# Kernel optimization log

Hardware: AMD Instinct MI355X
Metric: run time of the kernel (lower is better)

Reference implementation:

```python
import jax, jax.numpy as jnp
import numpy as np

N_NODES = 100000
N_EDGES = 1600000
IN_DIM, HID_DIM, OUT_DIM = 128, 128, 64


def setup_inputs() -> dict:
    key = jax.random.key(0)
    k1, k2, k3, k4, k5, k6, k7 = jax.random.split(key, 7)
    in_feat = jax.random.normal(k1, (N_NODES, IN_DIM), dtype=jnp.float32)
    src = jax.random.randint(k2, (N_EDGES,), 0, N_NODES, dtype=jnp.int32)
    dst = jax.random.randint(k3, (N_EDGES,), 0, N_NODES, dtype=jnp.int32)
    # GraphConv params (Glorot-style scale)
    W1 = jax.random.normal(k4, (IN_DIM, HID_DIM), dtype=jnp.float32) * (2.0 / (IN_DIM + HID_DIM)) ** 0.5
    b1 = jnp.zeros((HID_DIM,), dtype=jnp.float32)
    W2 = jax.random.normal(k5, (HID_DIM, OUT_DIM), dtype=jnp.float32) * (2.0 / (HID_DIM + OUT_DIM)) ** 0.5
    b2 = jnp.zeros((OUT_DIM,), dtype=jnp.float32)
    return {"in_feat": in_feat, "W1": W1, "b1": b1, "W2": W2, "b2": b2, "src": src, "dst": dst}


def _graph_conv(x, W, b, src, dst, inv_sqrt_out, inv_sqrt_in):
    # DGL GraphConv, norm='both': D_out^{-1/2} on source, sum-aggregate, D_in^{-1/2} on dest
    x = x * inv_sqrt_out[:, None]              # [N, d]
    msg = x[src]                               # gather: [E, d]
    agg = jax.ops.segment_sum(msg, dst, num_segments=x.shape[0])  # scatter-add: [N, d]
    agg = agg * inv_sqrt_in[:, None]
    return agg @ W + b


def reference(in_feat, W1, b1, W2, b2, src, dst):
    N = in_feat.shape[0]
    ones = jnp.ones(src.shape[0], dtype=in_feat.dtype)
    deg_out = jax.ops.segment_sum(ones, src, num_segments=N)
    deg_in = jax.ops.segment_sum(ones, dst, num_segments=N)
    # clamp degree to >= 1 (DGL behavior) before inverse sqrt
    inv_sqrt_out = jnp.maximum(deg_out, 1.0) ** -0.5
    inv_sqrt_in = jnp.maximum(deg_in, 1.0) ** -0.5
    h = _graph_conv(in_feat, W1, b1, src, dst, inv_sqrt_out, inv_sqrt_in)
    h = jax.nn.relu(h)
    h = _graph_conv(h, W2, b2, src, dst, inv_sqrt_out, inv_sqrt_in)
    return h
```

## Files before the change

### kernel.cpp

```cpp
#include <hip/hip_runtime.h>

#define N_NODES 100000
#define N_EDGES 1600000
#define IN_DIM 128
#define HID_DIM 128
#define OUT_DIM 64

#define NB 391
#define GRIDB 256
#define EPB (N_EDGES / GRIDB)

typedef unsigned short ushort_t;
typedef unsigned int uint_t;
typedef __attribute__((ext_vector_type(8))) short bf16x8;
typedef __attribute__((ext_vector_type(4))) float f32x4;

__device__ __forceinline__ float blo(uint_t u) { return __uint_as_float(u << 16); }
__device__ __forceinline__ float bhi(uint_t u) { return __uint_as_float(u & 0xFFFF0000u); }
__device__ __forceinline__ uint_t f2b(float f) {
    uint_t u = __float_as_uint(f);
    uint_t r = u + 0x7FFFu + ((u >> 16) & 1u);
    return r >> 16;
}
__device__ __forceinline__ uint_t pk2(float a, float b) { return f2b(a) | (f2b(b) << 16); }


__global__ __launch_bounds__(256) void histdeg_k(const int* __restrict__ src,
                                                 const int* __restrict__ dst,
                                                 int* __restrict__ dego,
                                                 int* __restrict__ bucketTot) {
    __shared__ int h[NB];
    int t = threadIdx.x, blk = blockIdx.x;
    for (int j = t; j < NB; j += 256) h[j] = 0;
    __syncthreads();
    int e0 = blk * EPB;
    for (int i = e0 + t; i < e0 + EPB; i += 256) {
        atomicAdd(&h[dst[i] >> 8], 1);
        atomicAdd(&dego[src[i]], 1);
    }
    __syncthreads();
    for (int j = t; j < NB; j += 256)
        if (h[j]) atomicAdd(&bucketTot[j], h[j]);
}


__global__ __launch_bounds__(512) void bscan_k(const int* __restrict__ bucketTot,
                                               int* __restrict__ bucketOfs,
                                               int* __restrict__ fill) {
    __shared__ int s[512];
    int t = threadIdx.x;
    int v = (t < NB) ? bucketTot[t] : 0;
    s[t] = v;
    __syncthreads();
    for (int off = 1; off < 512; off <<= 1) {
        int x = (t >= off) ? s[t - off] : 0;
        __syncthreads();
        s[t] += x;
        __syncthreads();
    }
    if (t < NB) {
        int e = s[t] - v;
        bucketOfs[t] = e;
        fill[t] = e;
    }
    if (t == 0) bucketOfs[NB] = N_EDGES;
}


__global__ __launch_bounds__(256) void scat_k(const int* __restrict__ src,
                                              const int* __restrict__ dst,
                                              int* __restrict__ fill,
                                              uint_t* __restrict__ ebuf) {
    __shared__ int lcnt[NB];
    __shared__ int base[NB];
    __shared__ int lpos[NB];
    int t = threadIdx.x, blk = blockIdx.x;
    for (int j = t; j < NB; j += 256) {
        lcnt[j] = 0;
        lpos[j] = 0;
    }
    __syncthreads();
    int e0 = blk * EPB;
    for (int i = e0 + t; i < e0 + EPB; i += 256) atomicAdd(&lcnt[dst[i] >> 8], 1);
    __syncthreads();
    for (int j = t; j < NB; j += 256) {
        int c = lcnt[j];
        base[j] = c ? atomicAdd(&fill[j], c) : 0;
    }
    __syncthreads();
    for (int i = e0 + t; i < e0 + EPB; i += 256) {
        int d = dst[i];
        int b = d >> 8;
        int slot = atomicAdd(&lpos[b], 1);
        ebuf[base[b] + slot] = (uint_t)src[i] | ((uint_t)(d & 255) << 17);
    }
}


__global__ __launch_bounds__(256) void fin_k(const uint_t* __restrict__ ebuf,
                                             const int* __restrict__ bucketOfs,
                                             int* __restrict__ ofs,
                                             int* __restrict__ esrc) {
    __shared__ int cnt[256];
    __shared__ int s[256];
    __shared__ int fil[256];
    int b = blockIdx.x, t = threadIdx.x;
    int e0 = bucketOfs[b];
    int e1 = bucketOfs[b + 1];
    cnt[t] = 0;
    __syncthreads();
    for (int i = e0 + t; i < e1; i += 256) atomicAdd(&cnt[ebuf[i] >> 17], 1);
    __syncthreads();
    int c = cnt[t];
    s[t] = c;
    __syncthreads();
    for (int off = 1; off < 256; off <<= 1) {
        int x = (t >= off) ? s[t - off] : 0;
        __syncthreads();
        s[t] += x;
        __syncthreads();
    }
    int excl = s[t] - c;
    int node = b * 256 + t;
    if (node < N_NODES) ofs[node] = e0 + excl;
    if (b == NB - 1 && t == 0) ofs[N_NODES] = N_EDGES;
    fil[t] = excl;
    __syncthreads();
    for (int i = e0 + t; i < e1; i += 256) {
        uint_t u = ebuf[i];
        int slot = atomicAdd(&fil[u >> 17], 1);
        esrc[e0 + slot] = (int)(u & 0x1FFFFu);
    }
}


__global__ __launch_bounds__(256) void prepw_k(const float* __restrict__ x,
                                               const int* __restrict__ dego,
                                               ushort_t* __restrict__ xs,
                                               const float* __restrict__ W1,
                                               const float* __restrict__ W2,
                                               ushort_t* __restrict__ Wf1,
                                               ushort_t* __restrict__ Wf2) {
    constexpr int NB_PREP = N_NODES * 16 / 256;
    if ((int)blockIdx.x < NB_PREP) {
        int gid = blockIdx.x * 256 + threadIdx.x;
        int row = gid >> 4;
        float s = rsqrtf(fmaxf((float)dego[row], 1.0f));
        const float4* xp = (const float4*)x + (size_t)gid * 2;
        float4 va = xp[0], vb = xp[1];
        ((uint4*)xs)[gid] = make_uint4(pk2(va.x * s, va.y * s), pk2(va.z * s, va.w * s),
                                       pk2(vb.x * s, vb.y * s), pk2(vb.z * s, vb.w * s));
        return;
    }
    int gid = (blockIdx.x - NB_PREP) * 256 + threadIdx.x;
    const float* W;
    ushort_t* Wf;
    int BN;
    if (gid < HID_DIM * 16) {
        W = W1; Wf = Wf1; BN = HID_DIM;
    } else {
        gid -= HID_DIM * 16;
        if (gid >= OUT_DIM * 16) return;
        W = W2; Wf = Wf2; BN = OUT_DIM;
    }
    int l = gid & 63;
    int kc = (gid >> 6) & 3;
    int nt = gid >> 8;
    int col = nt * 16 + (l & 15);
    int k0 = kc * 32 + (l >> 4) * 8;
    uint_t r[4];
    #pragma unroll
    for (int p = 0; p < 4; ++p)
        r[p] = pk2(W[(size_t)(k0 + 2 * p) * BN + col], W[(size_t)(k0 + 2 * p + 1) * BN + col]);
    ((uint4*)Wf)[gid] = make_uint4(r[0], r[1], r[2], r[3]);
}

#define ACC8(v)                                         \
    acc[0] += blo(v.x); acc[1] += bhi(v.x);             \
    acc[2] += blo(v.y); acc[3] += bhi(v.y);             \
    acc[4] += blo(v.z); acc[5] += bhi(v.z);             \
    acc[6] += blo(v.w); acc[7] += bhi(v.w);


__global__ __launch_bounds__(256) void agg128_k(const ushort_t* __restrict__ xs,
                                                const int* __restrict__ esrc,
                                                const int* __restrict__ ofs,
                                                ushort_t* __restrict__ a) {
    int wid = (blockIdx.x * 256 + threadIdx.x) >> 6;
    int lane = threadIdx.x & 63;
    int q = lane >> 4, li = lane & 15;
    int beg = ofs[wid], end = ofs[wid + 1];
    float acc[8];
    #pragma unroll
    for (int i = 0; i < 8; ++i) acc[i] = 0.f;

    for (int j = beg; j < end; j += 64) {
        int m = end - j;
        if (m > 64) m = 64;
        int idx = (lane < m) ? esrc[j + lane] : 0;
        for (int t = 0; 4 * t < m; t += 4) {
            int e0 = 4 * t + q, e1 = e0 + 4, e2 = e0 + 8, e3 = e0 + 12;
            int s0 = __shfl(idx, e0 & 63);
            int s1 = __shfl(idx, e1 & 63);
            int s2 = __shfl(idx, e2 & 63);
            int s3 = __shfl(idx, e3 & 63);
            uint4 v0 = *(const uint4*)(xs + (size_t)s0 * 128 + li * 8);
            uint4 v1 = *(const uint4*)(xs + (size_t)s1 * 128 + li * 8);
            uint4 v2 = *(const uint4*)(xs + (size_t)s2 * 128 + li * 8);
            uint4 v3 = *(const uint4*)(xs + (size_t)s3 * 128 + li * 8);
            if (e0 < m) { ACC8(v0) }
            if (e1 < m) { ACC8(v1) }
            if (e2 < m) { ACC8(v2) }
            if (e3 < m) { ACC8(v3) }
        }
    }
    #pragma unroll
    for (int i = 0; i < 8; ++i) acc[i] += __shfl(acc[i], lane ^ 16);
    #pragma unroll
    for (int i = 0; i < 8; ++i) acc[i] += __shfl(acc[i], lane ^ 32);

    if (lane < 16) {
        float sc = rsqrtf(fmaxf((float)(end - beg), 1.0f));
        *(uint4*)(a + (size_t)wid * 128 + li * 8) =
            make_uint4(pk2(acc[0] * sc, acc[1] * sc), pk2(acc[2] * sc, acc[3] * sc),
                       pk2(acc[4] * sc, acc[5] * sc), pk2(acc[6] * sc, acc[7] * sc));
    }
}


__global__ __launch_bounds__(256) void mgemm12_k(const ushort_t* __restrict__ A,
                                                 const ushort_t* __restrict__ Wf1,
                                                 const ushort_t* __restrict__ Wf2,
                                                 const float* __restrict__ b1,
                                                 const int* __restrict__ dego,
                                                 ushort_t* __restrict__ ys) {
    __shared__ ushort_t Hs[4][16][136];
    int wv = threadIdx.x >> 6;
    int l = threadIdx.x & 63;
    int r0 = (blockIdx.x * 4 + wv) * 16;
    if (r0 >= N_NODES) return;
    int q = l >> 4, li = l & 15;

    const ushort_t* ap = A + (size_t)(r0 + li) * 128 + q * 8;
    bf16x8 af[4];
    #pragma unroll
    for (int kc = 0; kc < 4; ++kc) af[kc] = *(const bf16x8*)(ap + kc * 32);

    f32x4 acc[8];
    #pragma unroll
    for (int nt = 0; nt < 8; ++nt) acc[nt] = (f32x4){0.f, 0.f, 0.f, 0.f};

    #pragma unroll
    for (int kc = 0; kc < 4; ++kc) {
        #pragma unroll
        for (int nt = 0; nt < 8; ++nt) {
            bf16x8 bfr = *(const bf16x8*)(Wf1 + ((size_t)(nt * 4 + kc) * 64 + l) * 8);
            acc[nt] = __builtin_amdgcn_mfma_f32_16x16x32_bf16(af[kc], bfr, acc[nt], 0, 0, 0);
        }
    }

    #pragma unroll
    for (int nt = 0; nt < 8; ++nt) {
        float bv = b1[nt * 16 + li];
        #pragma unroll
        for (int j = 0; j < 4; ++j) {
            float x = fmaxf(acc[nt][j] + bv, 0.0f);
            Hs[wv][q * 4 + j][nt * 16 + li] = (ushort_t)f2b(x);
        }
    }

    bf16x8 hf[4];
    #pragma unroll
    for (int kc = 0; kc < 4; ++kc)
        hf[kc] = *(const bf16x8*)&Hs[wv][li][kc * 32 + q * 8];

    f32x4 acc2[4];
    #pragma unroll
    for (int nt = 0; nt < 4; ++nt) acc2[nt] = (f32x4){0.f, 0.f, 0.f, 0.f};

    #pragma unroll
    for (int kc = 0; kc < 4; ++kc) {
        #pragma unroll
        for (int nt = 0; nt < 4; ++nt) {
            bf16x8 bfr = *(const bf16x8*)(Wf2 + ((size_t)(nt * 4 + kc) * 64 + l) * 8);
            acc2[nt] = __builtin_amdgcn_mfma_f32_16x16x32_bf16(hf[kc], bfr, acc2[nt], 0, 0, 0);
        }
    }

    int orow = r0 + q * 4;
    float os[4];
    #pragma unroll
    for (int j = 0; j < 4; ++j) os[j] = rsqrtf(fmaxf((float)dego[orow + j], 1.0f));
    #pragma unroll
    for (int nt = 0; nt < 4; ++nt) {
        #pragma unroll
        for (int j = 0; j < 4; ++j) {
            ys[(size_t)(orow + j) * 64 + nt * 16 + li] = (ushort_t)f2b(acc2[nt][j] * os[j]);
        }
    }
}


__global__ __launch_bounds__(256) void agg64_k(const ushort_t* __restrict__ ys,
                                               const int* __restrict__ esrc,
                                               const int* __restrict__ ofs,
                                               const float* __restrict__ b2,
                                               float* __restrict__ out) {
    int wid = (blockIdx.x * 256 + threadIdx.x) >> 6;
    int lane = threadIdx.x & 63;
    int og = lane >> 3, li = lane & 7;
    int beg = ofs[wid], end = ofs[wid + 1];
    float acc[8];
    #pragma unroll
    for (int i = 0; i < 8; ++i) acc[i] = 0.f;

    for (int j = beg; j < end; j += 64) {
        int m = end - j;
        if (m > 64) m = 64;
        int idx = (lane < m) ? esrc[j + lane] : 0;
        for (int t = 0; 8 * t < m; t += 2) {
            int e0 = 8 * t + og, e1 = e0 + 8;
            int s0 = __shfl(idx, e0 & 63);
            int s1 = __shfl(idx, e1 & 63);
            uint4 v0 = *(const uint4*)(ys + (size_t)s0 * 64 + li * 8);
            uint4 v1 = *(const uint4*)(ys + (size_t)s1 * 64 + li * 8);
            if (e0 < m) { ACC8(v0) }
            if (e1 < m) { ACC8(v1) }
        }
    }
    #pragma unroll
    for (int i = 0; i < 8; ++i) acc[i] += __shfl(acc[i], lane ^ 8);
    #pragma unroll
    for (int i = 0; i < 8; ++i) acc[i] += __shfl(acc[i], lane ^ 16);
    #pragma unroll
    for (int i = 0; i < 8; ++i) acc[i] += __shfl(acc[i], lane ^ 32);

    if (lane < 8) {
        float sc = rsqrtf(fmaxf((float)(end - beg), 1.0f));
        float4 ba = *(const float4*)(b2 + li * 8);
        float4 bb = *(const float4*)(b2 + li * 8 + 4);
        float* op = out + (size_t)wid * 64 + li * 8;
        *(float4*)op = make_float4(acc[0] * sc + ba.x, acc[1] * sc + ba.y,
                                   acc[2] * sc + ba.z, acc[3] * sc + ba.w);
        *(float4*)(op + 4) = make_float4(acc[4] * sc + bb.x, acc[5] * sc + bb.y,
                                         acc[6] * sc + bb.z, acc[7] * sc + bb.w);
    }
}

extern "C" void kernel_launch(void* const* d_in, const int* in_sizes, int n_in,
                              void* d_out, int out_size, void* d_ws, size_t ws_size,
                              hipStream_t stream) {
    const float* in_feat = (const float*)d_in[0];
    const float* W1 = (const float*)d_in[1];
    const float* b1 = (const float*)d_in[2];
    const float* W2 = (const float*)d_in[3];
    const float* b2 = (const float*)d_in[4];
    const int* src = (const int*)d_in[5];
    const int* dst = (const int*)d_in[6];
    float* out = (float*)d_out;

    char* w = (char*)d_ws;
    int* dego = (int*)w;       w += (size_t)N_NODES * 4;
    int* bucketTot = (int*)w;  w += 392 * 4;
    int* fill = (int*)w;       w += 392 * 4;
    int* bucketOfs = (int*)w;  w += 400 * 4;
    int* ofs = (int*)w;        w += (size_t)(N_NODES + 4) * 4;
    uint_t* ebuf = (uint_t*)w; w += (size_t)N_EDGES * 4;
    int* esrc = (int*)w;       w += (size_t)N_EDGES * 4;
    ushort_t* Wf1 = (ushort_t*)w; w += (size_t)HID_DIM * 16 * 16;
    ushort_t* Wf2 = (ushort_t*)w; w += (size_t)OUT_DIM * 16 * 16;
    ushort_t* bufA = (ushort_t*)w; w += (size_t)N_NODES * HID_DIM * 2;
    ushort_t* bufB = (ushort_t*)w; w += (size_t)N_NODES * HID_DIM * 2;

    hipMemsetAsync(dego, 0, (size_t)(N_NODES + 392) * 4, stream);

    histdeg_k<<<GRIDB, 256, 0, stream>>>(src, dst, dego, bucketTot);
    bscan_k<<<1, 512, 0, stream>>>(bucketTot, bucketOfs, fill);
    scat_k<<<GRIDB, 256, 0, stream>>>(src, dst, fill, ebuf);
    fin_k<<<NB, 256, 0, stream>>>(ebuf, bucketOfs, ofs, esrc);

    prepw_k<<<N_NODES * 16 / 256 + 12, 256, 0, stream>>>(in_feat, dego, bufA, W1, W2, Wf1, Wf2);

    agg128_k<<<N_NODES / 4, 256, 0, stream>>>(bufA, esrc, ofs, bufB);

    mgemm12_k<<<(N_NODES / 16 + 3) / 4, 256, 0, stream>>>(bufB, Wf1, Wf2, b1, dego, bufA);

    agg64_k<<<N_NODES / 4, 256, 0, stream>>>(bufA, esrc, ofs, b2, out);
}
```

Baseline: 274.6 us.

## Replace global atomic out-degree count with bucketed source sort in LDS

Out-degree is no longer computed with 1.6M scattered global atomics into dego. Edges are now also bucketed by src>>8 in the histogram and scatter passes, each edge writing a one-byte low-index entry into a new sbuf. Extra blocks in the finalize kernel then count degrees per bucket with shared-memory atomics. This removes contended global atomics and the large memset, at the cost of a second bucket histogram, a second scan, extra scatter writes and more finalize blocks.

```diff
diff --git a/kernel.cpp b/kernel.cpp
--- a/kernel.cpp
+++ b/kernel.cpp
@@ -12,6 +12,7 @@
 
 typedef unsigned short ushort_t;
 typedef unsigned int uint_t;
+typedef unsigned char uchar_t;
 typedef __attribute__((ext_vector_type(8))) short bf16x8;
 typedef __attribute__((ext_vector_type(4))) float f32x4;
 
@@ -27,26 +28,32 @@
 
 __global__ __launch_bounds__(256) void histdeg_k(const int* __restrict__ src,
                                                  const int* __restrict__ dst,
-                                                 int* __restrict__ dego,
-                                                 int* __restrict__ bucketTot) {
-    __shared__ int h[NB];
+                                                 int* __restrict__ bucketTot,
+                                                 int* __restrict__ bucketTotS) {
+    __shared__ int hd[NB];
+    __shared__ int hs[NB];
     int t = threadIdx.x, blk = blockIdx.x;
-    for (int j = t; j < NB; j += 256) h[j] = 0;
+    for (int j = t; j < NB; j += 256) { hd[j] = 0; hs[j] = 0; }
     __syncthreads();
     int e0 = blk * EPB;
     for (int i = e0 + t; i < e0 + EPB; i += 256) {
-        atomicAdd(&h[dst[i] >> 8], 1);
-        atomicAdd(&dego[src[i]], 1);
-    }
-    __syncthreads();
-    for (int j = t; j < NB; j += 256)
-        if (h[j]) atomicAdd(&bucketTot[j], h[j]);
+        atomicAdd(&hd[dst[i] >> 8], 1);
+        atomicAdd(&hs[src[i] >> 8], 1);
+    }
+    __syncthreads();
+    for (int j = t; j < NB; j += 256) {
+        if (hd[j]) atomicAdd(&bucketTot[j], hd[j]);
+        if (hs[j]) atomicAdd(&bucketTotS[j], hs[j]);
+    }
 }
 
 
 __global__ __launch_bounds__(512) void bscan_k(const int* __restrict__ bucketTot,
+                                               const int* __restrict__ bucketTotS,
                                                int* __restrict__ bucketOfs,
-                                               int* __restrict__ fill) {
+                                               int* __restrict__ fill,
+                                               int* __restrict__ bucketOfsS,
+                                               int* __restrict__ fillS) {
     __shared__ int s[512];
     int t = threadIdx.x;
     int v = (t < NB) ? bucketTot[t] : 0;
@@ -64,49 +71,94 @@
         fill[t] = e;
     }
     if (t == 0) bucketOfs[NB] = N_EDGES;
+    __syncthreads();
+    int v2 = (t < NB) ? bucketTotS[t] : 0;
+    s[t] = v2;
+    __syncthreads();
+    for (int off = 1; off < 512; off <<= 1) {
+        int x = (t >= off) ? s[t - off] : 0;
+        __syncthreads();
+        s[t] += x;
+        __syncthreads();
+    }
+    if (t < NB) {
+        int e = s[t] - v2;
+        bucketOfsS[t] = e;
+        fillS[t] = e;
+    }
+    if (t == 0) bucketOfsS[NB] = N_EDGES;
 }
 
 
 __global__ __launch_bounds__(256) void scat_k(const int* __restrict__ src,
                                               const int* __restrict__ dst,
                                               int* __restrict__ fill,
-                                              uint_t* __restrict__ ebuf) {
+                                              int* __restrict__ fillS,
+                                              uint_t* __restrict__ ebuf,
+                                              uchar_t* __restrict__ sbuf) {
     __shared__ int lcnt[NB];
     __shared__ int base[NB];
     __shared__ int lpos[NB];
+    __shared__ int lcntS[NB];
+    __shared__ int baseS[NB];
+    __shared__ int lposS[NB];
     int t = threadIdx.x, blk = blockIdx.x;
     for (int j = t; j < NB; j += 256) {
-        lcnt[j] = 0;
-        lpos[j] = 0;
+        lcnt[j] = 0; lpos[j] = 0; lcntS[j] = 0; lposS[j] = 0;
     }
     __syncthreads();
     int e0 = blk * EPB;
-    for (int i = e0 + t; i < e0 + EPB; i += 256) atomicAdd(&lcnt[dst[i] >> 8], 1);
+    for (int i = e0 + t; i < e0 + EPB; i += 256) {
+        atomicAdd(&lcnt[dst[i] >> 8], 1);
+        atomicAdd(&lcntS[src[i] >> 8], 1);
+    }
     __syncthreads();
     for (int j = t; j < NB; j += 256) {
         int c = lcnt[j];
         base[j] = c ? atomicAdd(&fill[j], c) : 0;
+        int cs = lcntS[j];
+        baseS[j] = cs ? atomicAdd(&fillS[j], cs) : 0;
     }
     __syncthreads();
     for (int i = e0 + t; i < e0 + EPB; i += 256) {
-        int d = dst[i];
+        int sv = src[i], d = dst[i];
         int b = d >> 8;
         int slot = atomicAdd(&lpos[b], 1);
-        ebuf[base[b] + slot] = (uint_t)src[i] | ((uint_t)(d & 255) << 17);
-    }
-}
-
-
-__global__ __launch_bounds__(256) void fin_k(const uint_t* __restrict__ ebuf,
-                                             const int* __restrict__ bucketOfs,
-                                             int* __restrict__ ofs,
-                                             int* __restrict__ esrc) {
+        ebuf[base[b] + slot] = (uint_t)sv | ((uint_t)(d & 255) << 17);
+        int bs = sv >> 8;
+        int slotS = atomicAdd(&lposS[bs], 1);
+        sbuf[baseS[bs] + slotS] = (uchar_t)(sv & 255);
+    }
+}
+
+
+__global__ __launch_bounds__(256) void finx_k(const uint_t* __restrict__ ebuf,
+                                              const uchar_t* __restrict__ sbuf,
+                                              const int* __restrict__ bucketOfs,
+                                              const int* __restrict__ bucketOfsS,
+                                              int* __restrict__ ofs,
+                                              int* __restrict__ esrc,
+                                              int* __restrict__ dego) {
     __shared__ int cnt[256];
     __shared__ int s[256];
     __shared__ int fil[256];
-    int b = blockIdx.x, t = threadIdx.x;
-    int e0 = bucketOfs[b];
-    int e1 = bucketOfs[b + 1];
+    int t = threadIdx.x;
+    int blk = blockIdx.x;
+
+    if (blk >= NB) {
+        int b = blk - NB;
+        int e0 = bucketOfsS[b], e1 = bucketOfsS[b + 1];
+        cnt[t] = 0;
+        __syncthreads();
+        for (int i = e0 + t; i < e1; i += 256) atomicAdd(&cnt[sbuf[i]], 1);
+        __syncthreads();
+        int node = b * 256 + t;
+        if (node < N_NODES) dego[node] = cnt[t];
+        return;
+    }
+
+    int b = blk;
+    int e0 = bucketOfs[b], e1 = bucketOfs[b + 1];
     cnt[t] = 0;
     __syncthreads();
     for (int i = e0 + t; i < e1; i += 256) atomicAdd(&cnt[ebuf[i] >> 17], 1);
@@ -360,24 +412,29 @@
     float* out = (float*)d_out;
 
     char* w = (char*)d_ws;
-    int* dego = (int*)w;       w += (size_t)N_NODES * 4;
-    int* bucketTot = (int*)w;  w += 392 * 4;
-    int* fill = (int*)w;       w += 392 * 4;
-    int* bucketOfs = (int*)w;  w += 400 * 4;
-    int* ofs = (int*)w;        w += (size_t)(N_NODES + 4) * 4;
-    uint_t* ebuf = (uint_t*)w; w += (size_t)N_EDGES * 4;
-    int* esrc = (int*)w;       w += (size_t)N_EDGES * 4;
+    int* bucketTot = (int*)w;   w += 392 * 4;
+    int* bucketTotS = (int*)w;  w += 392 * 4;
+    int* fill = (int*)w;        w += 392 * 4;
+    int* fillS = (int*)w;       w += 392 * 4;
+    int* bucketOfs = (int*)w;   w += 400 * 4;
+    int* bucketOfsS = (int*)w;  w += 400 * 4;
+    int* dego = (int*)w;        w += (size_t)(N_NODES + 8) * 4;
+    int* ofs = (int*)w;         w += (size_t)(N_NODES + 8) * 4;
+    uint_t* ebuf = (uint_t*)w;  w += (size_t)N_EDGES * 4;
+    int* esrc = (int*)w;        w += (size_t)N_EDGES * 4;
+    uchar_t* sbuf = (uchar_t*)w; w += (size_t)N_EDGES;
+    w += (16 - ((size_t)w & 15)) & 15;
     ushort_t* Wf1 = (ushort_t*)w; w += (size_t)HID_DIM * 16 * 16;
     ushort_t* Wf2 = (ushort_t*)w; w += (size_t)OUT_DIM * 16 * 16;
     ushort_t* bufA = (ushort_t*)w; w += (size_t)N_NODES * HID_DIM * 2;
     ushort_t* bufB = (ushort_t*)w; w += (size_t)N_NODES * HID_DIM * 2;
 
-    hipMemsetAsync(dego, 0, (size_t)(N_NODES + 392) * 4, stream);
-
-    histdeg_k<<<GRIDB, 256, 0, stream>>>(src, dst, dego, bucketTot);
-    bscan_k<<<1, 512, 0, stream>>>(bucketTot, bucketOfs, fill);
-    scat_k<<<GRIDB, 256, 0, stream>>>(src, dst, fill, ebuf);
-    fin_k<<<NB, 256, 0, stream>>>(ebuf, bucketOfs, ofs, esrc);
+    hipMemsetAsync(bucketTot, 0, 2 * 392 * 4, stream);
+
+    histdeg_k<<<GRIDB, 256, 0, stream>>>(src, dst, bucketTot, bucketTotS);
+    bscan_k<<<1, 512, 0, stream>>>(bucketTot, bucketTotS, bucketOfs, fill, bucketOfsS, fillS);
+    scat_k<<<GRIDB, 256, 0, stream>>>(src, dst, fill, fillS, ebuf, sbuf);
+    finx_k<<<2 * NB, 256, 0, stream>>>(ebuf, sbuf, bucketOfs, bucketOfsS, ofs, esrc, dego);
 
     prepw_k<<<N_NODES * 16 / 256 + 12, 256, 0, stream>>>(in_feat, dego, bufA, W1, W2, Wf1, Wf2);
 
```

After: 231.8 us, median of 2. 15.6% less time.
